# Kernel tuning notes

Hardware: AMD Instinct MI355X
Metric: run time of the kernel (lower is better)

## Reference

```python
import jax, jax.numpy as jnp
import numpy as np

B, NV, NS, L = 32, 2048, 512, 64
FEAT, SEM, HID, ATT, DM = 1024, 512, 512, 512, 512


def setup_inputs() -> dict:
    key = jax.random.key(0)
    ks = jax.random.split(key, 14)
    s = lambda k, sh: jax.random.normal(k, sh, dtype=jnp.float32) * 0.02
    return {
        "query": jax.random.normal(ks[0], (B, 1, HID), dtype=jnp.float32),
        "visual_features": jax.random.normal(ks[1], (B, NV, FEAT), dtype=jnp.float32),
        "semantic_features": jax.random.normal(ks[2], (B, NS, SEM), dtype=jnp.float32),
        "patient_info": jax.random.normal(ks[3], (B, L, DM), dtype=jnp.float32),
        "W1v": s(ks[4], (HID, ATT)),
        "W2v": s(ks[5], (FEAT, ATT)),
        "vv": s(ks[6], (ATT, 1)),
        "W3": s(ks[7], (DM, ATT)),
        "b3": jnp.zeros((ATT,), dtype=jnp.float32),
        "W1s": s(ks[8], (HID, ATT)),
        "W2s": s(ks[9], (SEM, ATT)),
        "vs": s(ks[10], (ATT, 1)),
        "W": s(ks[11], (FEAT + SEM, FEAT)),
        "bW": jnp.zeros((FEAT,), dtype=jnp.float32),
    }


def reference(query, visual_features, semantic_features, patient_info,
              W1v, W2v, vv, W3, b3, W1s, W2s, vs, W, bW):
    # mean over patient sequence, project: [B,1,ATT]
    pinfo = jnp.mean(patient_info, axis=1, keepdims=True) @ W3 + b3
    q_v = query @ W1v          # [B,1,ATT]
    # visual branch
    v_scores = jnp.tanh(q_v + visual_features @ W2v + pinfo) @ vv  # [B,NV,1]
    v_attn = jax.nn.softmax(v_scores, axis=1)
    # semantic branch
    q_s = query @ W1s
    s_scores = jnp.tanh(q_s + semantic_features @ W2s + pinfo) @ vs  # [B,NS,1]
    s_attn = jax.nn.softmax(s_scores, axis=1)
    ctx = jnp.concatenate([
        jnp.sum(visual_features * v_attn, axis=1),    # [B,FEAT]
        jnp.sum(semantic_features * s_attn, axis=1),  # [B,SEM]
    ], axis=1) @ W + bW
    return ctx, v_attn, s_attn
```

## Files before the change

### kernel.cpp

```cpp
#include <hip/hip_runtime.h>

typedef float f32x4 __attribute__((ext_vector_type(4)));
typedef short short8 __attribute__((ext_vector_type(8)));

#define B_    32
#define NV_   2048
#define NS_   512
#define L_    64
#define FEAT_ 1024
#define SEM_  512
#define HID_  512
#define ATT_  512
#define DM_   512

#define FENCE asm volatile("" ::: "memory")

__device__ __forceinline__ unsigned int f2bf_pk(float lo, float hi) {
  unsigned int ul = (__float_as_uint(lo) + 0x8000u) >> 16;
  unsigned int uh = (__float_as_uint(hi) + 0x8000u) & 0xffff0000u;
  return uh | ul;
}

__device__ __forceinline__ unsigned short f2bf(float f) {
  return (unsigned short)((__float_as_uint(f) + 0x8000u) >> 16);
}

__device__ __forceinline__ float fast_tanh(float x) {
  float e = __expf(2.f * x);
  return 1.f - 2.f * __builtin_amdgcn_rcpf(e + 1.f);
}

__device__ __forceinline__ void gload16(const void* g, void* l) {
  __builtin_amdgcn_global_load_lds(
      (const __attribute__((address_space(1))) unsigned char*)g,
      (__attribute__((address_space(3))) unsigned char*)l, 16, 0, 0);
}

__global__ __launch_bounds__(256) void k_qp(const float* __restrict__ query,
                                            const float* __restrict__ pat,
                                            const float* __restrict__ W1v,
                                            const float* __restrict__ W1s,
                                            const float* __restrict__ W3,
                                            const float* __restrict__ b3,
                                            float* __restrict__ qpv,
                                            float* __restrict__ qps) {
  __shared__ float pmL[DM_];
  const int t = threadIdx.x;
  const int b = blockIdx.x >> 1;
  for (int d = t; d < DM_; d += 256) {
    float s = 0.f;
    for (int l = 0; l < L_; ++l) s += pat[(b * L_ + l) * DM_ + d];
    pmL[d] = s * (1.f / 64.f);
  }
  __syncthreads();
  const int a = (blockIdx.x & 1) * 256 + t;
  float pi = b3[a];
  for (int d = 0; d < DM_; ++d) pi += pmL[d] * W3[d * ATT_ + a];
  float qv = 0.f, qs = 0.f;
  for (int h = 0; h < HID_; ++h) {
    float q = query[b * HID_ + h];
    qv += q * W1v[h * ATT_ + a];
    qs += q * W1s[h * ATT_ + a];
  }
  qpv[b * ATT_ + a] = qv + pi;
  qps[b * ATT_ + a] = qs + pi;
}

__global__ __launch_bounds__(256) void k_swz2(const float* __restrict__ W2v,
                                              const float* __restrict__ W2s,
                                              unsigned short* __restrict__ outV,
                                              unsigned short* __restrict__ outS) {
  int idx = blockIdx.x * 256 + threadIdx.x;
  const float* src;
  unsigned short* dst;
  if (idx < FEAT_ * ATT_) {
    src = W2v; dst = outV;
  } else {
    idx -= FEAT_ * ATT_;
    if (idx >= SEM_ * ATT_) return;
    src = W2s; dst = outS;
  }
  int k = idx >> 9, c = idx & 511;
  int kc = k >> 5, kr = k & 31, q = kr >> 3, j = kr & 7;
  int cb = c >> 4, n = c & 15;
  dst[(kc * 32 + cb) * 512 + q * 128 + n * 8 + j] = f2bf(src[idx]);
}

__global__ __launch_bounds__(256, 2) void k_scores_fused(
    const float* __restrict__ X, const unsigned short* __restrict__ Wt,
    const float* __restrict__ qp, const float* __restrict__ vvec,
    float* __restrict__ score, int K, int rows_per_batch) {
  __shared__ __align__(16) float AsF[5 * 2048];
  const int t = threadIdx.x;
  const int lane = t & 63, wave = t >> 6;
  const int quad = lane >> 4, l15 = lane & 15;
  const int row0 = blockIdx.x * 64;
  const int b = row0 / rows_per_batch;
  const int nk = K >> 5;

  const int g_hi = lane >> 3, g_lo = lane & 7;
  const int sub = g_lo ^ (g_hi & 7);
  const int kofs = (sub >> 1) * 8 + (sub & 1) * 4;
  const float* gsrc0 = X + (size_t)(row0 + wave * 16 + g_hi) * K + kofs;
  const float* gsrc1 = X + (size_t)(row0 + wave * 16 + 8 + g_hi) * K + kofs;

  const int swz = (l15 & 7) << 4;
  const int ro0 = (l15 * 128 + quad * 32) ^ swz;
  const int ro1 = (l15 * 128 + quad * 32 + 16) ^ swz;

  const char* gB = (const char*)Wt + (size_t)wave * 8192 + lane * 16;

  const f32x4 zero = {0.f, 0.f, 0.f, 0.f};
  f32x4 acc[4][8];
#pragma unroll
  for (int a = 0; a < 4; ++a)
#pragma unroll
    for (int cb = 0; cb < 8; ++cb) acc[a][cb] = zero;

#pragma unroll
  for (int p = 0; p < 4; ++p) {
    char* d = (char*)AsF + p * 8192 + wave * 2048;
    gload16(gsrc0 + (size_t)p * 32, d);
    gload16(gsrc1 + (size_t)p * 32, d + 1024);
  }
  asm volatile("s_waitcnt vmcnt(6)" ::: "memory");

  for (int kc = 0; kc < nk; ++kc) {
    short8 bfr[8];
    const char* gBk = gB + (size_t)kc * 32768;
#pragma unroll
    for (int cb = 0; cb < 8; ++cb)
      bfr[cb] = *(const short8*)(gBk + cb * 1024);

    FENCE;
    __builtin_amdgcn_s_barrier();
    FENCE;

    {
      const int kn = (kc + 4 < nk) ? kc + 4 : nk - 1;
      char* d = (char*)AsF + ((kc + 4) % 5) * 8192 + wave * 2048;
      gload16(gsrc0 + (size_t)kn * 32, d);
      gload16(gsrc1 + (size_t)kn * 32, d + 1024);
    }
    FENCE;

    const char* bufR = (const char*)AsF + (kc % 5) * 8192;
#pragma unroll
    for (int a = 0; a < 4; ++a) {
      f32x4 lo = *(const f32x4*)(bufR + a * 2048 + ro0);
      f32x4 hi = *(const f32x4*)(bufR + a * 2048 + ro1);
      uint4 v;
      v.x = f2bf_pk(lo.x, lo.y);
      v.y = f2bf_pk(lo.z, lo.w);
      v.z = f2bf_pk(hi.x, hi.y);
      v.w = f2bf_pk(hi.z, hi.w);
      short8 af = (short8&)v;
#pragma unroll
      for (int cb = 0; cb < 8; ++cb)
        acc[a][cb] = __builtin_amdgcn_mfma_f32_16x16x32_bf16(af, bfr[cb], acc[a][cb], 0, 0, 0);
    }
  }

  float qv_[8], vw_[8];
#pragma unroll
  for (int cb = 0; cb < 8; ++cb) {
    int col = wave * 128 + cb * 16 + l15;
    qv_[cb] = qp[b * ATT_ + col];
    vw_[cb] = vvec[col];
  }
#pragma unroll
  for (int a = 0; a < 4; ++a) {
#pragma unroll
    for (int rr = 0; rr < 4; ++rr) {
      float s = 0.f;
#pragma unroll
      for (int cb = 0; cb < 8; ++cb)
        s += fast_tanh(acc[a][cb][rr] + qv_[cb]) * vw_[cb];
      s += __shfl_xor(s, 1);
      s += __shfl_xor(s, 2);
      s += __shfl_xor(s, 4);
      s += __shfl_xor(s, 8);
      if (l15 == 0) atomicAdd(&score[row0 + a * 16 + quad * 4 + rr], s);
    }
  }
}

__global__ __launch_bounds__(256) void k_softmax2(const float* __restrict__ scores_v,
                                                  const float* __restrict__ scores_s,
                                                  float* __restrict__ v_attn,
                                                  float* __restrict__ s_attn) {
  __shared__ float sm[4];
  const int bb = blockIdx.x, t = threadIdx.x;
  const float* s;
  float* dst;
  int N;
  if (bb < 32) { s = scores_v + (size_t)bb * NV_; dst = v_attn + (size_t)bb * NV_; N = NV_; }
  else         { s = scores_s + (size_t)(bb - 32) * NS_; dst = s_attn + (size_t)(bb - 32) * NS_; N = NS_; }
  float m = -1e30f;
  for (int i = t; i < N; i += 256) m = fmaxf(m, s[i]);
  for (int k = 32; k; k >>= 1) m = fmaxf(m, __shfl_xor(m, k));
  if ((t & 63) == 0) sm[t >> 6] = m;
  __syncthreads();
  m = fmaxf(fmaxf(sm[0], sm[1]), fmaxf(sm[2], sm[3]));
  __syncthreads();
  float sum = 0.f;
  for (int i = t; i < N; i += 256) sum += __expf(s[i] - m);
  for (int k = 32; k; k >>= 1) sum += __shfl_xor(sum, k);
  if ((t & 63) == 0) sm[t >> 6] = sum;
  __syncthreads();
  sum = sm[0] + sm[1] + sm[2] + sm[3];
  float inv = 1.f / sum;
  for (int i = t; i < N; i += 256) dst[i] = __expf(s[i] - m) * inv;
}

__global__ __launch_bounds__(256) void k_wsum2(const float* __restrict__ vf,
                                               const float* __restrict__ sf,
                                               const float* __restrict__ v_attn,
                                               const float* __restrict__ s_attn,
                                               float* __restrict__ ctx_pre) {
  const int b = blockIdx.x, y = blockIdx.y, t = threadIdx.x;
  const float* feats;
  const float* attn;
  int N, F, colOff, r0;
  if (y < 8) { feats = vf; attn = v_attn; N = NV_; F = FEAT_; colOff = 0;     r0 = y * 256; }
  else       { feats = sf; attn = s_attn; N = NS_; F = SEM_;  colOff = 1024;  r0 = (y - 8) * 256; }
  const int c4 = t * 4;
  if (c4 >= F) return;
  const float* fb = feats + ((size_t)b * N + r0) * F;
  const float* ab = attn + (size_t)b * N + r0;
  float4 acc = {0.f, 0.f, 0.f, 0.f};
#pragma unroll 4
  for (int r = 0; r < 256; ++r) {
    float a = ab[r];
    float4 v = *(const float4*)(fb + (size_t)r * F + c4);
    acc.x += a * v.x; acc.y += a * v.y; acc.z += a * v.z; acc.w += a * v.w;
  }
  float* dst = ctx_pre + b * 1536 + colOff + c4;
  atomicAdd(dst + 0, acc.x);
  atomicAdd(dst + 1, acc.y);
  atomicAdd(dst + 2, acc.z);
  atomicAdd(dst + 3, acc.w);
}

__global__ __launch_bounds__(256) void k_final(const float* __restrict__ cp,
                                               const float* __restrict__ W,
                                               const float* __restrict__ bW,
                                               float* __restrict__ out) {
  int b = blockIdx.x, oc = blockIdx.y, t = threadIdx.x;
  int o = oc * 256 + t;
  float acc = bW[o];
  const float* c = cp + b * 1536;
  for (int k = 0; k < 1536; ++k) acc += c[k] * W[k * FEAT_ + o];
  out[b * FEAT_ + o] = acc;
}

extern "C" void kernel_launch(void* const* d_in, const int* in_sizes, int n_in,
                              void* d_out, int out_size, void* d_ws, size_t ws_size,
                              hipStream_t stream) {
  const float* query = (const float*)d_in[0];
  const float* vf    = (const float*)d_in[1];
  const float* sf    = (const float*)d_in[2];
  const float* pat   = (const float*)d_in[3];
  const float* W1v   = (const float*)d_in[4];
  const float* W2v   = (const float*)d_in[5];
  const float* vv    = (const float*)d_in[6];
  const float* W3    = (const float*)d_in[7];
  const float* b3    = (const float*)d_in[8];
  const float* W1s   = (const float*)d_in[9];
  const float* W2s   = (const float*)d_in[10];
  const float* vs    = (const float*)d_in[11];
  const float* W     = (const float*)d_in[12];
  const float* bW    = (const float*)d_in[13];
  float* out = (float*)d_out;

  char* ws = (char*)d_ws;
  float* scores_v = (float*)(ws);
  float* scores_s = (float*)(ws + 262144);
  float* ctx_pre  = (float*)(ws + 327680);
  float* qpv      = (float*)(ws + 524288);
  float* qps      = (float*)(ws + 589824);
  unsigned short* Wtv = (unsigned short*)(ws + 655360);
  unsigned short* Wts = (unsigned short*)(ws + 655360 + 1048576);

  hipMemsetAsync(d_ws, 0, 524288, stream);

  k_swz2<<<(FEAT_ * ATT_ + SEM_ * ATT_) / 256, 256, 0, stream>>>(W2v, W2s, Wtv, Wts);
  k_qp<<<64, 256, 0, stream>>>(query, pat, W1v, W1s, W3, b3, qpv, qps);

  float* v_attn = out + B_ * FEAT_;
  float* s_attn = out + B_ * FEAT_ + B_ * NV_;

  k_scores_fused<<<(B_ * NV_) / 64, 256, 0, stream>>>(vf, Wtv, qpv, vv, scores_v, FEAT_, NV_);
  k_scores_fused<<<(B_ * NS_) / 64, 256, 0, stream>>>(sf, Wts, qps, vs, scores_s, SEM_, NS_);
  k_softmax2<<<64, 256, 0, stream>>>(scores_v, scores_s, v_attn, s_attn);
  k_wsum2<<<dim3(B_, 10), 256, 0, stream>>>(vf, sf, v_attn, s_attn, ctx_pre);
  k_final<<<dim3(B_, 4), 256, 0, stream>>>(ctx_pre, W, bW, out);
}
```

Measured before the change: 659.1 us.

## Stage bf16 A and B tiles through double-buffered LDS with register prefetch

```diff
diff --git a/kernel.cpp b/kernel.cpp
--- a/kernel.cpp
+++ b/kernel.cpp
@@ -90,7 +90,8 @@
     const float* __restrict__ X, const unsigned short* __restrict__ Wt,
     const float* __restrict__ qp, const float* __restrict__ vvec,
     float* __restrict__ score, int K, int rows_per_batch) {
-  __shared__ __align__(16) float AsF[5 * 2048];
+  __shared__ __align__(16) char LdsA[2 * 4096];
+  __shared__ __align__(16) char LdsB[2 * 32768];
   const int t = threadIdx.x;
   const int lane = t & 63, wave = t >> 6;
   const int quad = lane >> 4, l15 = lane & 15;
@@ -98,17 +99,12 @@
   const int b = row0 / rows_per_batch;
   const int nk = K >> 5;
 
-  const int g_hi = lane >> 3, g_lo = lane & 7;
-  const int sub = g_lo ^ (g_hi & 7);
-  const int kofs = (sub >> 1) * 8 + (sub & 1) * 4;
-  const float* gsrc0 = X + (size_t)(row0 + wave * 16 + g_hi) * K + kofs;
-  const float* gsrc1 = X + (size_t)(row0 + wave * 16 + 8 + g_hi) * K + kofs;
-
-  const int swz = (l15 & 7) << 4;
-  const int ro0 = (l15 * 128 + quad * 32) ^ swz;
-  const int ro1 = (l15 * 128 + quad * 32 + 16) ^ swz;
-
-  const char* gB = (const char*)Wt + (size_t)wave * 8192 + lane * 16;
+  const int r = t >> 2, q_ = t & 3;
+  const float* gA = X + (size_t)(row0 + r) * K + q_ * 8;
+  const int awOff = (r >> 4) * 1024 + q_ * 256 + (((r & 15) ^ (q_ << 1)) << 4);
+  const int arOff = quad * 256 + ((l15 ^ (quad << 1)) << 4);
+  const char* gBsrc = (const char*)Wt + (size_t)wave * 8192 + lane * 16;
+  const int brOff = wave * 8192 + lane * 16;
 
   const f32x4 zero = {0.f, 0.f, 0.f, 0.f};
   f32x4 acc[4][8];
@@ -117,49 +113,88 @@
 #pragma unroll
     for (int cb = 0; cb < 8; ++cb) acc[a][cb] = zero;
 
-#pragma unroll
-  for (int p = 0; p < 4; ++p) {
-    char* d = (char*)AsF + p * 8192 + wave * 2048;
-    gload16(gsrc0 + (size_t)p * 32, d);
-    gload16(gsrc1 + (size_t)p * 32, d + 1024);
-  }
-  asm volatile("s_waitcnt vmcnt(6)" ::: "memory");
-
-  for (int kc = 0; kc < nk; ++kc) {
-    short8 bfr[8];
-    const char* gBk = gB + (size_t)kc * 32768;
-#pragma unroll
-    for (int cb = 0; cb < 8; ++cb)
-      bfr[cb] = *(const short8*)(gBk + cb * 1024);
-
-    FENCE;
-    __builtin_amdgcn_s_barrier();
-    FENCE;
-
-    {
-      const int kn = (kc + 4 < nk) ? kc + 4 : nk - 1;
-      char* d = (char*)AsF + ((kc + 4) % 5) * 8192 + wave * 2048;
-      gload16(gsrc0 + (size_t)kn * 32, d);
-      gload16(gsrc1 + (size_t)kn * 32, d + 1024);
-    }
-    FENCE;
-
-    const char* bufR = (const char*)AsF + (kc % 5) * 8192;
-#pragma unroll
-    for (int a = 0; a < 4; ++a) {
-      f32x4 lo = *(const f32x4*)(bufR + a * 2048 + ro0);
-      f32x4 hi = *(const f32x4*)(bufR + a * 2048 + ro1);
-      uint4 v;
-      v.x = f2bf_pk(lo.x, lo.y);
-      v.y = f2bf_pk(lo.z, lo.w);
-      v.z = f2bf_pk(hi.x, hi.y);
-      v.w = f2bf_pk(hi.z, hi.w);
-      short8 af = (short8&)v;
-#pragma unroll
-      for (int cb = 0; cb < 8; ++cb)
-        acc[a][cb] = __builtin_amdgcn_mfma_f32_16x16x32_bf16(af, bfr[cb], acc[a][cb], 0, 0, 0);
-    }
-  }
+  f32x4 T0a = *(const f32x4*)(gA);
+  f32x4 T0b = *(const f32x4*)(gA + 4);
+  FENCE;
+  {
+    char* dst = LdsB + wave * 8192;
+#pragma unroll
+    for (int i = 0; i < 8; ++i) gload16(gBsrc + i * 1024, dst + i * 1024);
+  }
+  FENCE;
+  f32x4 A1a = *(const f32x4*)(gA + 32),  A1b = *(const f32x4*)(gA + 36);
+  f32x4 A2a = *(const f32x4*)(gA + 64),  A2b = *(const f32x4*)(gA + 68);
+  f32x4 A3a = *(const f32x4*)(gA + 96),  A3b = *(const f32x4*)(gA + 100);
+  f32x4 A0a = *(const f32x4*)(gA + 128), A0b = *(const f32x4*)(gA + 132);
+  FENCE;
+  {
+    uint4 w;
+    w.x = f2bf_pk(T0a.x, T0a.y); w.y = f2bf_pk(T0a.z, T0a.w);
+    w.z = f2bf_pk(T0b.x, T0b.y); w.w = f2bf_pk(T0b.z, T0b.w);
+    *(uint4*)(LdsA + awOff) = w;
+  }
+  asm volatile("s_waitcnt lgkmcnt(0)\n\ts_waitcnt vmcnt(8)" ::: "memory");
+  __builtin_amdgcn_s_barrier();
+  FENCE;
+
+#define STEP(KC, Pa, Pb)                                                       \
+  {                                                                            \
+    const int kc = (KC);                                                       \
+    \
+    uint4 w;                                                                   \
+    w.x = f2bf_pk(Pa.x, Pa.y); w.y = f2bf_pk(Pa.z, Pa.w);                      \
+    w.z = f2bf_pk(Pb.x, Pb.y); w.w = f2bf_pk(Pb.z, Pb.w);                      \
+    *(uint4*)(LdsA + ((kc + 1) & 1) * 4096 + awOff) = w;                       \
+    FENCE;                                                                     \
+        \
+    {                                                                          \
+      const int kn = (kc + 1 < nk) ? kc + 1 : nk - 1;                          \
+      const char* src = gBsrc + (size_t)kn * 32768;                            \
+      char* dst = LdsB + ((kc + 1) & 1) * 32768 + wave * 8192;                 \
+      _Pragma("unroll")                                                        \
+      for (int i = 0; i < 8; ++i) gload16(src + i * 1024, dst + i * 1024);     \
+    }                                                                          \
+    FENCE;                                                                     \
+                    \
+    {                                                                          \
+      const int kn5 = (kc + 5 < nk) ? kc + 5 : nk - 1;                         \
+      Pa = *(const f32x4*)(gA + (size_t)kn5 * 32);                             \
+      Pb = *(const f32x4*)(gA + (size_t)kn5 * 32 + 4);                         \
+    }                                                                          \
+    FENCE;                                                                     \
+       \
+    asm volatile("s_waitcnt lgkmcnt(0)\n\ts_waitcnt vmcnt(12)" ::: "memory");  \
+    __builtin_amdgcn_s_barrier();                                              \
+    FENCE;                                                                     \
+                                    \
+    {                                                                          \
+      const char* ab = LdsA + (kc & 1) * 4096;                                 \
+      const char* bb = LdsB + (kc & 1) * 32768;                                \
+      short8 af[4], bf8[8];                                                    \
+      _Pragma("unroll")                                                        \
+      for (int a = 0; a < 4; ++a) af[a] = *(const short8*)(ab + a * 1024 + arOff); \
+      _Pragma("unroll")                                                        \
+      for (int j = 0; j < 8; ++j) bf8[j] = *(const short8*)(bb + brOff + j * 1024); \
+      __builtin_amdgcn_s_setprio(1);                                           \
+      _Pragma("unroll")                                                        \
+      for (int a = 0; a < 4; ++a)                                              \
+        _Pragma("unroll")                                                      \
+        for (int j = 0; j < 8; ++j)                                            \
+          acc[a][j] = __builtin_amdgcn_mfma_f32_16x16x32_bf16(af[a], bf8[j], acc[a][j], 0, 0, 0); \
+      __builtin_amdgcn_s_setprio(0);                                           \
+    }                                                                          \
+    FENCE;                                                                     \
+    __builtin_amdgcn_s_barrier(); \
+    FENCE;                                                                     \
+  }
+
+  for (int kb = 0; kb < nk; kb += 4) {
+    STEP(kb + 0, A1a, A1b);
+    STEP(kb + 1, A2a, A2b);
+    STEP(kb + 2, A3a, A3b);
+    STEP(kb + 3, A0a, A0b);
+  }
+#undef STEP
 
   float qv_[8], vw_[8];
 #pragma unroll
```

Result: no change. 664.9 us (+0.9%).
